# Optimization experiments

Measured on AMD Instinct MI355X. Metric: run time of the kernel, lower is better.

## Reference

```python
import jax, jax.numpy as jnp
import numpy as np
import math

D_MODEL = 1024
N_HEADS = 16
D_K = D_MODEL // N_HEADS  # 64
NB_FEATURES = 256
EPS = 1e-6


def _create_projection_matrix(nb_features, d_k, rng):
    # Orthogonal blocks (rows of Q^T) scaled by chi-distributed row norms.
    nb_full_blocks = nb_features // d_k
    blocks = []
    for _ in range(nb_full_blocks):
        q, _ = np.linalg.qr(rng.standard_normal((d_k, d_k)))
        blocks.append(q.T)
    rem = nb_features - nb_full_blocks * d_k
    if rem > 0:
        q, _ = np.linalg.qr(rng.standard_normal((d_k, d_k)))
        blocks.append(q.T[:rem])
    mat = np.concatenate(blocks, axis=0)
    norms = np.linalg.norm(rng.standard_normal((nb_features, d_k)), axis=1)
    return jnp.asarray(mat * norms[:, None], dtype=jnp.float32)


def setup_inputs() -> dict:
    key = jax.random.key(0)
    ks = jax.random.split(key, 6)
    B, L = 4, 4096
    scale = 1.0 / math.sqrt(D_MODEL)
    return {
        "hidden_states": jax.random.normal(ks[0], (B, L, D_MODEL), dtype=jnp.float32),
        "attention_mask": jnp.ones((B, L), dtype=jnp.int32),
        "Wq": jax.random.normal(ks[1], (D_MODEL, D_MODEL), dtype=jnp.float32) * scale,
        "Wk": jax.random.normal(ks[2], (D_MODEL, D_MODEL), dtype=jnp.float32) * scale,
        "Wv": jax.random.normal(ks[3], (D_MODEL, D_MODEL), dtype=jnp.float32) * scale,
        "Wo": jax.random.normal(ks[4], (D_MODEL, D_MODEL), dtype=jnp.float32) * scale,
        "projection_matrix": _create_projection_matrix(NB_FEATURES, D_K, np.random.default_rng(0)),
    }


def _favor_features(x, proj):
    # x: [B,H,L,dk] -> phi: [B,H,L,m]; approximates softmax kernel (FAVOR+)
    data_normalizer = D_K ** (-0.25)
    ratio = NB_FEATURES ** (-0.5)
    projected = jnp.einsum("bhld,md->bhlm", data_normalizer * x, proj)
    norm_sq = jnp.sum(x * x, axis=-1, keepdims=True) * (data_normalizer ** 2) * 0.5
    projected_max = jax.lax.stop_gradient(jnp.max(projected, axis=-1, keepdims=True))
    return ratio * (jnp.exp(projected - projected_max - norm_sq) + EPS)


def reference(hidden_states, attention_mask, Wq, Wk, Wv, Wo, projection_matrix):
    B, L, _ = hidden_states.shape
    def split_heads(x):  # [B,L,D] -> [B,H,L,dk]
        return x.reshape(B, L, N_HEADS, D_K).transpose(0, 2, 1, 3)
    q = split_heads(hidden_states @ Wq.T)
    k = split_heads(hidden_states @ Wk.T)
    v = split_heads(hidden_states @ Wv.T)
    phi_q = _favor_features(q, projection_matrix)
    phi_k = _favor_features(k, projection_matrix)
    phi_k = phi_k * attention_mask[:, None, :, None].astype(phi_k.dtype)
    kv = jnp.einsum("bhlm,bhld->bhmd", phi_k, v)           # [B,H,m,dk]
    out = jnp.einsum("bhlm,bhmd->bhld", phi_q, kv)          # [B,H,L,dk]
    k_sum = jnp.sum(phi_k, axis=2)                           # [B,H,m]
    denom = jnp.einsum("bhlm,bhm->bhl", phi_q, k_sum)[..., None]
    out = out / jnp.maximum(denom, EPS)
    out = out.transpose(0, 2, 1, 3).reshape(B, L, D_MODEL)
    return out @ Wo.T
```

## Files before the change

kernel.cpp:

```cpp
#include <hip/hip_runtime.h>
#include <math.h>

#define B 4
#define L 4096
#define D 1024
#define H 16
#define DK 64
#define M 256
#define NTOK (B*L)
#define NCH 8
#define LC (L/NCH)

#define DNORM 0.35355339059327373f
#define HALF_DN2 0.0625f
#define RATIO 0.0625f

typedef _Float16 f16x8 __attribute__((ext_vector_type(8)));
typedef _Float16 f16x2 __attribute__((ext_vector_type(2)));
typedef float f32x4 __attribute__((ext_vector_type(4)));
typedef unsigned u32x4 __attribute__((ext_vector_type(4)));

#define SWZ(col, l) ((col) * 64 + (((l) & 7) | ((((((l) >> 3)) ^ (col)) & 7) << 3)))

__device__ __forceinline__ void gload16(const void* g, void* l) {
    __builtin_amdgcn_global_load_lds((const __attribute__((address_space(1))) unsigned*)g,
                                     (__attribute__((address_space(3))) unsigned*)l, 16, 0, 0);
}

__global__ __launch_bounds__(256) void cast_f32_f16(const float* __restrict__ in,
                                                    _Float16* __restrict__ out, int n8) {
    int i = blockIdx.x * 256 + threadIdx.x;
    if (i >= n8) return;
    const float4* p = (const float4*)(in + (size_t)i * 8);
    float4 a = p[0], b = p[1];
    f16x8 o;
    o[0] = (_Float16)a.x; o[1] = (_Float16)a.y; o[2] = (_Float16)a.z; o[3] = (_Float16)a.w;
    o[4] = (_Float16)b.x; o[5] = (_Float16)b.y; o[6] = (_Float16)b.z; o[7] = (_Float16)b.w;
    *(f16x8*)(out + (size_t)i * 8) = o;
}

__global__ __launch_bounds__(256) void cast_w4(const float* __restrict__ Wk,
                                               const float* __restrict__ Wv,
                                               const float* __restrict__ Wq,
                                               const float* __restrict__ Wo,
                                               _Float16* __restrict__ Wall) {
    const int y = blockIdx.y;
    const float* src = (y == 0) ? Wk : (y == 1) ? Wv : (y == 2) ? Wq : Wo;
    const int i = blockIdx.x * 256 + threadIdx.x;
    const float4* p = (const float4*)(src + (size_t)i * 8);
    float4 a = p[0], b = p[1];
    f16x8 o;
    o[0] = (_Float16)a.x; o[1] = (_Float16)a.y; o[2] = (_Float16)a.z; o[3] = (_Float16)a.w;
    o[4] = (_Float16)b.x; o[5] = (_Float16)b.y; o[6] = (_Float16)b.z; o[7] = (_Float16)b.w;
    *(f16x8*)(Wall + (size_t)y * 1048576 + (size_t)i * 8) = o;
}

__global__ __launch_bounds__(256) void cast_P_frag(const float* __restrict__ P,
                                                   _Float16* __restrict__ Phf) {
    const int t = threadIdx.x;
#pragma unroll
    for (int i = 0; i < 8; i++) {
        const int c = t + i * 256;
        const int f = c >> 6, lane2 = c & 63;
        const int nf = f >> 1, kh = f & 1;
        const int fr = lane2 & 15, kq2 = lane2 >> 4;
        const float* src = P + (nf * 16 + fr) * 64 + kh * 32 + kq2 * 8;
        f16x8 o;
#pragma unroll
        for (int j = 0; j < 8; j++) o[j] = (_Float16)src[j];
        *(f16x8*)(Phf + (size_t)c * 8) = o;
    }
}

template <typename CT>
__global__ __launch_bounds__(256) void gemm_f16(const _Float16* __restrict__ A,
                                                const _Float16* __restrict__ W,
                                                CT* __restrict__ C,
                                                int N, int K) {
    __shared__ _Float16 As[128 * 64];
    __shared__ _Float16 Bs[128 * 64];
    const int t    = threadIdx.x;
    const int lane = t & 63;
    const int w    = t >> 6;
    const int wr   = w >> 1, wc = w & 1;

    const int nwg = gridDim.x * gridDim.y;
    int lid = blockIdx.y * gridDim.x + blockIdx.x;
    lid = (lid & 7) * (nwg >> 3) + (lid >> 3);
    const int bx = lid % gridDim.x, by = lid / gridDim.x;
    const int brow = by * 128, bcol = bx * 128;

    const int fr = lane & 15;
    const int kq = lane >> 4;

    int srow[4], soff[4];
#pragma unroll
    for (int i = 0; i < 4; i++) {
        const int c = t + i * 256;
        srow[i] = c >> 3;
        soff[i] = ((c & 7) ^ ((c >> 3) & 7)) * 8;
    }

    f32x4 acc[4][4];
#pragma unroll
    for (int i = 0; i < 4; i++)
#pragma unroll
        for (int j = 0; j < 4; j++) acc[i][j] = (f32x4){0.f, 0.f, 0.f, 0.f};

    for (int k0 = 0; k0 < K; k0 += 64) {
        __syncthreads();
#pragma unroll
        for (int i = 0; i < 4; i++) {
            const int c = t + i * 256;
            gload16(A + (size_t)(brow + srow[i]) * K + k0 + soff[i], As + c * 8);
            gload16(W + (size_t)(bcol + srow[i]) * K + k0 + soff[i], Bs + c * 8);
        }
        __syncthreads();
#pragma unroll
        for (int kh = 0; kh < 2; kh++) {
            f16x8 af[4], bf[4];
#pragma unroll
            for (int mi = 0; mi < 4; mi++) {
                const int row = wr * 64 + mi * 16 + fr;
                af[mi] = *(const f16x8*)&As[row * 64 + (((kh * 4 + kq) ^ (row & 7)) << 3)];
            }
#pragma unroll
            for (int ni = 0; ni < 4; ni++) {
                const int row = wc * 64 + ni * 16 + fr;
                bf[ni] = *(const f16x8*)&Bs[row * 64 + (((kh * 4 + kq) ^ (row & 7)) << 3)];
            }
#pragma unroll
            for (int mi = 0; mi < 4; mi++)
#pragma unroll
                for (int ni = 0; ni < 4; ni++)
                    acc[mi][ni] = __builtin_amdgcn_mfma_f32_16x16x32_f16(af[mi], bf[ni], acc[mi][ni], 0, 0, 0);
        }
    }
#pragma unroll
    for (int mi = 0; mi < 4; mi++) {
#pragma unroll
        for (int ni = 0; ni < 4; ni++) {
            const int row = brow + wr * 64 + mi * 16 + kq * 4;
            const int col = bcol + wc * 64 + ni * 16 + fr;
#pragma unroll
            for (int r = 0; r < 4; r++)
                C[(size_t)(row + r) * N + col] = (CT)acc[mi][ni][r];
        }
    }
}

__global__ __launch_bounds__(256) void kv_kernel4(const _Float16* __restrict__ kvb,
                                                  const int* __restrict__ mask,
                                                  const _Float16* __restrict__ Phf,
                                                  float* __restrict__ kvpart,
                                                  float* __restrict__ kspart) {
    const int bh = blockIdx.y, b = bh >> 4, h = bh & 15;
    const int ch = blockIdx.x;
    const int t = threadIdx.x, lane = t & 63, w = t >> 6;
    const int fr = lane & 15, kq = lane >> 4;

    __shared__ _Float16 phis[256 * 64];
    __shared__ _Float16 vst[80 * 64];

    if (t < 128) {
        const int row = 64 + (t >> 3), off = (t & 7) * 8;
        const _Float16 val = (row == 64) ? (_Float16)1.0f : (_Float16)0.0f;
        f16x8 o = {val, val, val, val, val, val, val, val};
        *(f16x8*)&vst[row * 64 + off] = o;
    }
    __syncthreads();

    f32x4 acc[4][5];
#pragma unroll
    for (int mf = 0; mf < 4; mf++)
#pragma unroll
        for (int n2 = 0; n2 < 5; n2++) acc[mf][n2] = (f32x4){0.f, 0.f, 0.f, 0.f};

    const int rr = t & 31, seg = t >> 5;

    for (int tile = 0; tile < LC / 64; ++tile) {
        const int l0 = ch * LC + tile * 64;

        {
            const _Float16* v0 = kvb + (size_t)(b * L + l0 + 2 * rr) * 2048 + 1024 + h * DK + seg * 8;
            f16x8 a0 = *(const f16x8*)v0;
            f16x8 a1 = *(const f16x8*)(v0 + 2048);
#pragma unroll
            for (int j = 0; j < 8; j++) {
                const int d = seg * 8 + j;
                f16x2 pk = {a0[j], a1[j]};
                *(f16x2*)&vst[SWZ(d, 2 * rr)] = pk;
            }
        }

        const _Float16* krow = kvb + (size_t)(b * L + l0 + w * 16 + fr) * 2048 + h * DK + kq * 8;
        f16x8 ak0 = *(const f16x8*)krow;
        f16x8 ak1 = *(const f16x8*)(krow + 32);
        float ns = 0.f;
#pragma unroll
        for (int j = 0; j < 8; j++)
            ns += (float)ak0[j] * (float)ak0[j] + (float)ak1[j] * (float)ak1[j];
        ns += __shfl_xor(ns, 16);
        ns += __shfl_xor(ns, 32);
        ns *= HALF_DN2;

        f32x4 pr[16];
#pragma unroll
        for (int nf = 0; nf < 16; nf++) {
            f16x8 b0 = *(const f16x8*)&Phf[((size_t)(nf * 2 + 0) * 64 + lane) * 8];
            f16x8 b1 = *(const f16x8*)&Phf[((size_t)(nf * 2 + 1) * 64 + lane) * 8];
            f32x4 c = {0.f, 0.f, 0.f, 0.f};
            c = __builtin_amdgcn_mfma_f32_16x16x32_f16(ak0, b0, c, 0, 0, 0);
            c = __builtin_amdgcn_mfma_f32_16x16x32_f16(ak1, b1, c, 0, 0, 0);
            pr[nf] = c;
        }
        float mx[4] = {-1e30f, -1e30f, -1e30f, -1e30f};
#pragma unroll
        for (int nf = 0; nf < 16; nf++)
#pragma unroll
            for (int r = 0; r < 4; r++) {
                pr[nf][r] *= DNORM;
                mx[r] = fmaxf(mx[r], pr[nf][r]);
            }
#pragma unroll
        for (int r = 0; r < 4; r++) {
            mx[r] = fmaxf(mx[r], __shfl_xor(mx[r], 1));
            mx[r] = fmaxf(mx[r], __shfl_xor(mx[r], 2));
            mx[r] = fmaxf(mx[r], __shfl_xor(mx[r], 4));
            mx[r] = fmaxf(mx[r], __shfl_xor(mx[r], 8));
        }
        float sub[4], mkv[4];
#pragma unroll
        for (int r = 0; r < 4; r++) {
            sub[r] = mx[r] + __shfl(ns, kq * 4 + r);
            mkv[r] = (float)mask[b * L + l0 + w * 16 + kq * 4 + r];
        }
#pragma unroll
        for (int nf = 0; nf < 16; nf++) {
            const int col = nf * 16 + fr;
#pragma unroll
            for (int rp = 0; rp < 2; rp++) {
                const int row = w * 16 + kq * 4 + 2 * rp;
                float v0 = mkv[2 * rp]     * (RATIO * (__expf(pr[nf][2 * rp]     - sub[2 * rp])     + 1e-6f));
                float v1 = mkv[2 * rp + 1] * (RATIO * (__expf(pr[nf][2 * rp + 1] - sub[2 * rp + 1]) + 1e-6f));
                f16x2 pk = {(_Float16)v0, (_Float16)v1};
                *(f16x2*)&phis[SWZ(col, row)] = pk;
            }
        }
        __syncthreads();

        f16x8 bfr[5][2];
#pragma unroll
        for (int n2 = 0; n2 < 5; n2++)
#pragma unroll
            for (int ks = 0; ks < 2; ks++)
                bfr[n2][ks] = *(const f16x8*)&vst[SWZ(n2 * 16 + fr, ks * 32 + kq * 8)];
#pragma unroll
        for (int mf = 0; mf < 4; mf++) {
            const int m = w * 64 + mf * 16 + fr;
            f16x8 a0 = *(const f16x8*)&phis[SWZ(m, kq * 8)];
            f16x8 a1 = *(const f16x8*)&phis[SWZ(m, 32 + kq * 8)];
#pragma unroll
            for (int n2 = 0; n2 < 5; n2++) {
                acc[mf][n2] = __builtin_amdgcn_mfma_f32_16x16x32_f16(a0, bfr[n2][0], acc[mf][n2], 0, 0, 0);
                acc[mf][n2] = __builtin_amdgcn_mfma_f32_16x16x32_f16(a1, bfr[n2][1], acc[mf][n2], 0, 0, 0);
            }
        }
        __syncthreads();
    }

    float* kvp = kvpart + ((size_t)ch * 64 + bh) * M * DK;
    float* ksp = kspart + ((size_t)ch * 64 + bh) * M;
#pragma unroll
    for (int mf = 0; mf < 4; mf++) {
#pragma unroll
        for (int r = 0; r < 4; r++) {
            const int m = w * 64 + mf * 16 + kq * 4 + r;
#pragma unroll
            for (int n2 = 0; n2 < 4; n2++)
                kvp[(size_t)m * DK + n2 * 16 + fr] = acc[mf][n2][r];
            if (fr == 0) ksp[m] = acc[mf][4][r];
        }
    }
}

__global__ __launch_bounds__(256) void reduce_kvt2(const float* __restrict__ kvp,
                                                   const float* __restrict__ ksp,
                                                   _Float16* __restrict__ kvt) {
    const int dq = blockIdx.x, bh = blockIdx.y;
    const int t  = threadIdx.x;
    float s[16];
#pragma unroll
    for (int c = 0; c < 16; c++) s[c] = 0.f;
    for (int ch = 0; ch < NCH; ch++) {
        const float* src = kvp + (((size_t)ch * 64 + bh) * M + t) * DK + dq * 16;
#pragma unroll
        for (int c4 = 0; c4 < 4; c4++) {
            float4 v = *(const float4*)(src + c4 * 4);
            s[c4 * 4 + 0] += v.x; s[c4 * 4 + 1] += v.y;
            s[c4 * 4 + 2] += v.z; s[c4 * 4 + 3] += v.w;
        }
    }
    _Float16* dst = kvt + (size_t)bh * 20480;
    const int ks = t >> 5, kq = (t >> 3) & 3, j = t & 7;
#pragma unroll
    for (int c = 0; c < 16; c++)
        dst[((dq * 8 + ks) * 64 + kq * 16 + c) * 8 + j] = (_Float16)s[c];
    if (dq == 0) {
        float s64 = 0.f;
        for (int ch = 0; ch < NCH; ch++) s64 += ksp[((size_t)ch * 64 + bh) * M + t];
        dst[((4 * 8 + ks) * 64 + kq * 16 + 0) * 8 + j] = (_Float16)s64;
#pragma unroll
        for (int c = 1; c < 16; c++)
            dst[((4 * 8 + ks) * 64 + kq * 16 + c) * 8 + j] = (_Float16)0.f;
    }
}

__global__ __launch_bounds__(256) void out_kernel8(const _Float16* __restrict__ q,
                                                   const _Float16* __restrict__ Phf,
                                                   const _Float16* __restrict__ kvtf,
                                                   _Float16* __restrict__ ao) {
    const int nwg = gridDim.x * gridDim.y;
    int lid = blockIdx.y * gridDim.x + blockIdx.x;
    lid = (lid & 7) * (nwg >> 3) + (lid >> 3);
    const int bh = lid >> 6, lblk = lid & 63;
    const int b = bh >> 4, h = bh & 15;
    const int l0 = lblk * 64;
    const int t = threadIdx.x, lane = t & 63, w = t >> 6;
    const int fr = lane & 15, kq = lane >> 4;

    __shared__ _Float16 kvs[2560 * 8];

    {
        const _Float16* src = kvtf + (size_t)bh * 20480 + t * 8;
#pragma unroll
        for (int i = 0; i < 10; i++)
            gload16(src + i * 2048, kvs + t * 8 + i * 2048);
    }

    const int srcA = fr + 16 * ((2 * kq) & 3);
    const int srcB = fr + 16 * ((2 * kq + 1) & 3);
    const bool hi  = (kq & 2) != 0;

    const _Float16* qp = q + (size_t)(b * L + l0 + w * 16 + fr) * D + h * DK + kq * 8;
    f16x8 aq0 = *(const f16x8*)qp;
    f16x8 aq1 = *(const f16x8*)(qp + 32);
    float ns = 0.f;
#pragma unroll
    for (int j = 0; j < 8; j++)
        ns += (float)aq0[j] * (float)aq0[j] + (float)aq1[j] * (float)aq1[j];
    ns += __shfl_xor(ns, 16);
    ns += __shfl_xor(ns, 32);
    ns *= HALF_DN2;

    f32x4 pr[16];
#pragma unroll
    for (int nf = 0; nf < 16; nf++) {
        f16x8 a0 = *(const f16x8*)&Phf[((size_t)(nf * 2 + 0) * 64 + lane) * 8];
        f16x8 a1 = *(const f16x8*)&Phf[((size_t)(nf * 2 + 1) * 64 + lane) * 8];
        f32x4 c = {0.f, 0.f, 0.f, 0.f};
        c = __builtin_amdgcn_mfma_f32_16x16x32_f16(a0, aq0, c, 0, 0, 0);
        c = __builtin_amdgcn_mfma_f32_16x16x32_f16(a1, aq1, c, 0, 0, 0);
        pr[nf] = c;
    }
    float mx = -1e30f;
#pragma unroll
    for (int nf = 0; nf < 16; nf++)
#pragma unroll
        for (int r = 0; r < 4; r++) {
            pr[nf][r] *= DNORM;
            mx = fmaxf(mx, pr[nf][r]);
        }
    mx = fmaxf(mx, __shfl_xor(mx, 16));
    mx = fmaxf(mx, __shfl_xor(mx, 32));
    const float sub = mx + ns;

    unsigned pk_[16][2];
#pragma unroll
    for (int nf = 0; nf < 16; nf++) {
#pragma unroll
        for (int p = 0; p < 2; p++) {
            float v0 = RATIO * (__expf(pr[nf][2 * p]     - sub) + 1e-6f);
            float v1 = RATIO * (__expf(pr[nf][2 * p + 1] - sub) + 1e-6f);
            f16x2 pq = {(_Float16)v0, (_Float16)v1};
            pk_[nf][p] = __builtin_bit_cast(unsigned, pq);
        }
    }
    __syncthreads();

    f32x4 acc[5];
#pragma unroll
    for (int n2 = 0; n2 < 5; n2++) acc[n2] = (f32x4){0.f, 0.f, 0.f, 0.f};
#pragma unroll
    for (int ks = 0; ks < 8; ks++) {
        unsigned u0 = __shfl(pk_[2 * ks][0], srcA);
        unsigned u1 = __shfl(pk_[2 * ks][1], srcA);
        unsigned u2 = __shfl(pk_[2 * ks][0], srcB);
        unsigned u3 = __shfl(pk_[2 * ks][1], srcB);
        unsigned v0 = __shfl(pk_[2 * ks + 1][0], srcA);
        unsigned v1 = __shfl(pk_[2 * ks + 1][1], srcA);
        unsigned v2 = __shfl(pk_[2 * ks + 1][0], srcB);
        unsigned v3 = __shfl(pk_[2 * ks + 1][1], srcB);
        u32x4 wv;
        wv[0] = hi ? v0 : u0;
        wv[1] = hi ? v1 : u1;
        wv[2] = hi ? v2 : u2;
        wv[3] = hi ? v3 : u3;
        f16x8 af = __builtin_bit_cast(f16x8, wv);
#pragma unroll
        for (int n2 = 0; n2 < 5; n2++) {
            f16x8 bf = *(const f16x8*)&kvs[((n2 * 8 + ks) * 64 + lane) * 8];
            acc[n2] = __builtin_amdgcn_mfma_f32_16x16x32_f16(af, bf, acc[n2], 0, 0, 0);
        }
    }
#pragma unroll
    for (int r = 0; r < 4; r++) {
        float den = __shfl(acc[4][r], (lane & 48));
        float inv = 1.f / fmaxf(den, 1e-6f);
        const int row = l0 + w * 16 + kq * 4 + r;
        _Float16* dst = ao + (size_t)(b * L + row) * D + h * DK;
#pragma unroll
        for (int n2 = 0; n2 < 4; n2++)
            dst[n2 * 16 + fr] = (_Float16)(acc[n2][r] * inv);
    }
}

extern "C" void kernel_launch(void* const* d_in, const int* in_sizes, int n_in,
                              void* d_out, int out_size, void* d_ws, size_t ws_size,
                              hipStream_t stream) {
    (void)in_sizes; (void)n_in; (void)out_size; (void)ws_size;
    const float* X    = (const float*)d_in[0];
    const int*   mask = (const int*)d_in[1];
    const float* Wq   = (const float*)d_in[2];
    const float* Wk   = (const float*)d_in[3];
    const float* Wv   = (const float*)d_in[4];
    const float* Wo   = (const float*)d_in[5];
    const float* P    = (const float*)d_in[6];

    char* ws = (char*)d_ws;
    _Float16* Xh    = (_Float16*)ws;
    _Float16* kvb   = (_Float16*)(ws + 33554432);
    _Float16* attn  = (_Float16*)(ws + 33554432);
    _Float16* bufQ  = (_Float16*)(ws + 67108864);
    float* kvpart   = (float*)(ws + 100663296);
    float* kspart   = (float*)(ws + 134217728);
    _Float16* kvt   = (_Float16*)(ws + 134742016);
    _Float16* Wall  = (_Float16*)(ws + 137363456);
    _Float16* Phf   = (_Float16*)(ws + 145752064);
    float* out      = (float*)d_out;

    dim3 blk(256);
    hipLaunchKernelGGL(cast_f32_f16, dim3(8192), blk, 0, stream, X, Xh, 2097152);
    hipLaunchKernelGGL(cast_w4, dim3(512, 4), blk, 0, stream, Wk, Wv, Wq, Wo, Wall);
    hipLaunchKernelGGL(cast_P_frag, dim3(1), blk, 0, stream, P, Phf);

    hipLaunchKernelGGL((gemm_f16<_Float16>), dim3(16, 128), blk, 0, stream, Xh, Wall, kvb, 2048, D);

    hipLaunchKernelGGL(kv_kernel4, dim3(NCH, B * H), blk, 0, stream, kvb, mask, Phf, kvpart, kspart);
    hipLaunchKernelGGL(reduce_kvt2, dim3(4, 64), blk, 0, stream, kvpart, kspart, kvt);

    hipLaunchKernelGGL((gemm_f16<_Float16>), dim3(8, 128), blk, 0, stream, Xh, Wall + 2 * 1048576, bufQ, D, D);

    hipLaunchKernelGGL(out_kernel8, dim3(L / 64, B * H), blk, 0, stream, bufQ, Phf, kvt, attn);

    hipLaunchKernelGGL((gemm_f16<float>), dim3(8, 128), blk, 0, stream, attn, Wall + 3 * 1048576, out, D, D);
}
```

Baseline: 330.6 us.

## Replace 128x128 GEMM with double-buffered 256x256 tile, 8-wave pipelined kernel

```diff
diff --git a/kernel.cpp b/kernel.cpp
--- a/kernel.cpp
+++ b/kernel.cpp
@@ -73,80 +73,122 @@
 }
 
 template <typename CT>
-__global__ __launch_bounds__(256) void gemm_f16(const _Float16* __restrict__ A,
-                                                const _Float16* __restrict__ W,
-                                                CT* __restrict__ C,
-                                                int N, int K) {
-    __shared__ _Float16 As[128 * 64];
-    __shared__ _Float16 Bs[128 * 64];
-    const int t    = threadIdx.x;
+__global__ __launch_bounds__(512) void gemm256(const _Float16* __restrict__ A,
+                                               const _Float16* __restrict__ W,
+                                               CT* __restrict__ C,
+                                               int N, int K) {
+    __shared__ _Float16 As[2][256 * 64];
+    __shared__ _Float16 Bs[2][256 * 64];
+    const int t = threadIdx.x;
     const int lane = t & 63;
-    const int w    = t >> 6;
-    const int wr   = w >> 1, wc = w & 1;
+    const int wid = t >> 6;
+    const int wr = wid >> 2, wc = wid & 3;
+    const int fr = lane & 15, kq = lane >> 4;
 
     const int nwg = gridDim.x * gridDim.y;
     int lid = blockIdx.y * gridDim.x + blockIdx.x;
     lid = (lid & 7) * (nwg >> 3) + (lid >> 3);
     const int bx = lid % gridDim.x, by = lid / gridDim.x;
-    const int brow = by * 128, bcol = bx * 128;
-
-    const int fr = lane & 15;
-    const int kq = lane >> 4;
-
-    int srow[4], soff[4];
-#pragma unroll
-    for (int i = 0; i < 4; i++) {
-        const int c = t + i * 256;
-        srow[i] = c >> 3;
-        soff[i] = ((c & 7) ^ ((c >> 3) & 7)) * 8;
-    }
-
-    f32x4 acc[4][4];
-#pragma unroll
-    for (int i = 0; i < 4; i++)
+    const int brow = by * 256, bcol = bx * 256;
+
+    const int nt = K >> 6;
+
+    f32x4 acc[8][4];
+#pragma unroll
+    for (int i = 0; i < 8; i++)
 #pragma unroll
         for (int j = 0; j < 4; j++) acc[i][j] = (f32x4){0.f, 0.f, 0.f, 0.f};
 
-    for (int k0 = 0; k0 < K; k0 += 64) {
-        __syncthreads();
-#pragma unroll
-        for (int i = 0; i < 4; i++) {
-            const int c = t + i * 256;
-            gload16(A + (size_t)(brow + srow[i]) * K + k0 + soff[i], As + c * 8);
-            gload16(W + (size_t)(bcol + srow[i]) * K + k0 + soff[i], Bs + c * 8);
-        }
-        __syncthreads();
-#pragma unroll
-        for (int kh = 0; kh < 2; kh++) {
-            f16x8 af[4], bf[4];
-#pragma unroll
-            for (int mi = 0; mi < 4; mi++) {
-                const int row = wr * 64 + mi * 16 + fr;
-                af[mi] = *(const f16x8*)&As[row * 64 + (((kh * 4 + kq) ^ (row & 7)) << 3)];
-            }
-#pragma unroll
-            for (int ni = 0; ni < 4; ni++) {
-                const int row = wc * 64 + ni * 16 + fr;
-                bf[ni] = *(const f16x8*)&Bs[row * 64 + (((kh * 4 + kq) ^ (row & 7)) << 3)];
-            }
-#pragma unroll
-            for (int mi = 0; mi < 4; mi++)
-#pragma unroll
-                for (int ni = 0; ni < 4; ni++)
-                    acc[mi][ni] = __builtin_amdgcn_mfma_f32_16x16x32_f16(af[mi], bf[ni], acc[mi][ni], 0, 0, 0);
-        }
-    }
-#pragma unroll
-    for (int mi = 0; mi < 4; mi++) {
+    f16x8 af[4][2], bf[4][2];
+
+#define STAGE_PAIR(buf_, k0_, j_) { \
+    const int c_ = (j_) * 512 + t; \
+    const int srow_ = c_ >> 3; \
+    const int src_ = (c_ & 7) ^ (srow_ & 7); \
+    gload16(A + (size_t)(brow + srow_) * K + (k0_) + src_ * 8, &As[buf_][c_ * 8]); \
+    gload16(W + (size_t)(bcol + srow_) * K + (k0_) + src_ * 8, &Bs[buf_][c_ * 8]); }
+
+#define READ_A(buf_, mh_) { \
+    _Pragma("unroll") \
+    for (int mi = 0; mi < 4; mi++) { \
+        const int row_ = wr * 128 + (mh_) * 64 + mi * 16 + fr; \
+        af[mi][0] = *(const f16x8*)&As[buf_][row_ * 64 + ((kq ^ (row_ & 7)) << 3)]; \
+        af[mi][1] = *(const f16x8*)&As[buf_][row_ * 64 + (((4 + kq) ^ (row_ & 7)) << 3)]; \
+    } }
+
+#define READ_B2(buf_, nh_) { \
+    _Pragma("unroll") \
+    for (int ni = 0; ni < 2; ni++) { \
+        const int row_ = wc * 64 + ((nh_) * 2 + ni) * 16 + fr; \
+        bf[(nh_) * 2 + ni][0] = *(const f16x8*)&Bs[buf_][row_ * 64 + ((kq ^ (row_ & 7)) << 3)]; \
+        bf[(nh_) * 2 + ni][1] = *(const f16x8*)&Bs[buf_][row_ * 64 + (((4 + kq) ^ (row_ & 7)) << 3)]; \
+    } }
+
+#define MFMA_Q(mh_, nh_) { \
+    _Pragma("unroll") \
+    for (int mi = 0; mi < 4; mi++) \
+        _Pragma("unroll") \
+        for (int ni = 0; ni < 2; ni++) { \
+            acc[(mh_) * 4 + mi][(nh_) * 2 + ni] = __builtin_amdgcn_mfma_f32_16x16x32_f16( \
+                af[mi][0], bf[(nh_) * 2 + ni][0], acc[(mh_) * 4 + mi][(nh_) * 2 + ni], 0, 0, 0); \
+            acc[(mh_) * 4 + mi][(nh_) * 2 + ni] = __builtin_amdgcn_mfma_f32_16x16x32_f16( \
+                af[mi][1], bf[(nh_) * 2 + ni][1], acc[(mh_) * 4 + mi][(nh_) * 2 + ni], 0, 0, 0); \
+        } }
+
+#define WAIT_LGKM { asm volatile("s_waitcnt lgkmcnt(0)" ::: "memory"); __builtin_amdgcn_sched_barrier(0); }
+#define WAIT_VM2  { asm volatile("s_waitcnt vmcnt(2)" ::: "memory"); __builtin_amdgcn_sched_barrier(0); }
+#define BAR __builtin_amdgcn_s_barrier()
+
+    STAGE_PAIR(0, 0, 0);
+    STAGE_PAIR(0, 0, 1);
+    STAGE_PAIR(0, 0, 2);
+    STAGE_PAIR(0, 0, 3);
+    STAGE_PAIR(1, (nt > 1 ? 64 : 0), 0);
+    WAIT_VM2; BAR;
+
+    for (int tau = 0; tau < nt; ++tau) {
+        const int cur = tau & 1, nxt = cur ^ 1;
+        const int k1 = (tau + 1 < nt) ? (tau + 1) * 64 : 0;
+        const int k2 = (tau + 2 < nt) ? (tau + 2) * 64 : 0;
+        READ_A(cur, 0);
+        READ_B2(cur, 0);
+        STAGE_PAIR(nxt, k1, 1);
+        BAR; WAIT_LGKM;
+        __builtin_amdgcn_s_setprio(1); MFMA_Q(0, 0); __builtin_amdgcn_s_setprio(0);
+        BAR;
+        READ_B2(cur, 1);
+        STAGE_PAIR(nxt, k1, 2);
+        BAR; WAIT_LGKM;
+        __builtin_amdgcn_s_setprio(1); MFMA_Q(0, 1); __builtin_amdgcn_s_setprio(0);
+        BAR;
+        READ_A(cur, 1);
+        STAGE_PAIR(nxt, k1, 3);
+        BAR; WAIT_LGKM;
+        __builtin_amdgcn_s_setprio(1); MFMA_Q(1, 0); __builtin_amdgcn_s_setprio(0);
+        BAR;
+        __builtin_amdgcn_s_setprio(1); MFMA_Q(1, 1); __builtin_amdgcn_s_setprio(0);
+        STAGE_PAIR(cur, k2, 0);
+        WAIT_VM2; BAR;
+    }
+    asm volatile("s_waitcnt vmcnt(0)" ::: "memory");
+
+#pragma unroll
+    for (int mi = 0; mi < 8; mi++)
 #pragma unroll
         for (int ni = 0; ni < 4; ni++) {
-            const int row = brow + wr * 64 + mi * 16 + kq * 4;
+            const int row = brow + wr * 128 + mi * 16 + kq * 4;
             const int col = bcol + wc * 64 + ni * 16 + fr;
 #pragma unroll
             for (int r = 0; r < 4; r++)
                 C[(size_t)(row + r) * N + col] = (CT)acc[mi][ni][r];
         }
-    }
+#undef STAGE_PAIR
+#undef READ_A
+#undef READ_B2
+#undef MFMA_Q
+#undef WAIT_LGKM
+#undef WAIT_VM2
+#undef BAR
 }
 
 __global__ __launch_bounds__(256) void kv_kernel4(const _Float16* __restrict__ kvb,
@@ -409,8 +451,8 @@
         f16x8 af = __builtin_bit_cast(f16x8, wv);
 #pragma unroll
         for (int n2 = 0; n2 < 5; n2++) {
-            f16x8 bf = *(const f16x8*)&kvs[((n2 * 8 + ks) * 64 + lane) * 8];
-            acc[n2] = __builtin_amdgcn_mfma_f32_16x16x32_f16(af, bf, acc[n2], 0, 0, 0);
+            f16x8 bfv = *(const f16x8*)&kvs[((n2 * 8 + ks) * 64 + lane) * 8];
+            acc[n2] = __builtin_amdgcn_mfma_f32_16x16x32_f16(af, bfv, acc[n2], 0, 0, 0);
         }
     }
 #pragma unroll
@@ -454,14 +496,14 @@
     hipLaunchKernelGGL(cast_w4, dim3(512, 4), blk, 0, stream, Wk, Wv, Wq, Wo, Wall);
     hipLaunchKernelGGL(cast_P_frag, dim3(1), blk, 0, stream, P, Phf);
 
-    hipLaunchKernelGGL((gemm_f16<_Float16>), dim3(16, 128), blk, 0, stream, Xh, Wall, kvb, 2048, D);
+    hipLaunchKernelGGL((gemm256<_Float16>), dim3(8, 64), dim3(512), 0, stream, Xh, Wall, kvb, 2048, D);
 
     hipLaunchKernelGGL(kv_kernel4, dim3(NCH, B * H), blk, 0, stream, kvb, mask, Phf, kvpart, kspart);
     hipLaunchKernelGGL(reduce_kvt2, dim3(4, 64), blk, 0, stream, kvpart, kspart, kvt);
 
-    hipLaunchKernelGGL((gemm_f16<_Float16>), dim3(8, 128), blk, 0, stream, Xh, Wall + 2 * 1048576, bufQ, D, D);
+    hipLaunchKernelGGL((gemm256<_Float16>), dim3(4, 64), dim3(512), 0, stream, Xh, Wall + 2 * 1048576, bufQ, D, D);
 
     hipLaunchKernelGGL(out_kernel8, dim3(L / 64, B * H), blk, 0, stream, bufQ, Phf, kvt, attn);
 
-    hipLaunchKernelGGL((gemm_f16<float>), dim3(8, 128), blk, 0, stream, attn, Wall + 3 * 1048576, out, D, D);
-}
+    hipLaunchKernelGGL((gemm256<float>), dim3(4, 64), dim3(512), 0, stream, attn, Wall + 3 * 1048576, out, D, D);
+}
```

Result: faster. 299.0 us (-9.6%).
